# Kernel optimization log

Measured on AMD Instinct MI355X. Metric: run time of the kernel, lower is better.

Reference implementation:

```python
import jax, jax.numpy as jnp
import numpy as np

HEADS = 4


def rel_to_abs(x):
    """Convert relative logits [..., L, 2L-1] to absolute [..., L, L].
    out[..., i, j] = x[..., i, j - i + L - 1]."""
    L = x.shape[-2]
    idx = jnp.arange(L)[None, :] - jnp.arange(L)[:, None] + (L - 1)  # [L, L]
    idx = jnp.broadcast_to(idx, x.shape[:-1] + (L,))
    return jnp.take_along_axis(x, idx, axis=-1)


def setup_inputs() -> dict:
    key = jax.random.key(0)
    ks = jax.random.split(key, 5)
    b, c, h, w = 2, 256, 64, 64
    dh = c // HEADS
    return {
        "x": jax.random.normal(ks[0], (b, c, h, w), jnp.float32),
        "w_qkv": jax.random.normal(ks[1], (3 * c, c), jnp.float32) / np.float32(np.sqrt(c)),
        "w_out": jax.random.normal(ks[2], (c, c), jnp.float32) / np.float32(np.sqrt(c)),
        "rel_height": jax.random.normal(ks[3], (2 * h - 1, dh), jnp.float32),
        "rel_width": jax.random.normal(ks[4], (2 * w - 1, dh), jnp.float32),
    }


def reference(x, w_qkv, w_out, rel_height, rel_width):
    b, c, h, w = x.shape
    dh = c // HEADS
    N = h * w
    scale = dh ** -0.5

    # 1x1 conv == per-pixel matmul over channels
    qkv = jnp.einsum('bchw,oc->bohw', x, w_qkv)  # [b, 3c, h, w]
    q, k, v = jnp.split(qkv, 3, axis=1)

    def to_heads(t):  # [b, c, h, w] -> [b, H, N, dh]
        return t.reshape(b, HEADS, dh, N).transpose(0, 1, 3, 2)

    q = to_heads(q) * scale
    k = to_heads(k)
    v = to_heads(v)

    # content-content scores over spatial positions
    content = jnp.einsum('bnid,bnjd->bnij', q, k)  # [b, H, N, N]

    q5 = q.reshape(b, HEADS, h, w, dh)  # [b, H, x, y, dh]
    # width relative logits: [b,H,x,y,2w-1] -> abs -> [b,H,x,y,jw]
    rw = rel_to_abs(jnp.einsum('bnxyd,rd->bnxyr', q5, rel_width))
    # height relative logits on transposed spatial: [b,H,y,x,2h-1] -> [b,H,y,x,jh]
    rh = rel_to_abs(jnp.einsum('bnyxd,rd->bnyxr', q5.transpose(0, 1, 3, 2, 4), rel_height))

    logits = content.reshape(b, HEADS, h, w, h, w)
    logits = logits + rw[:, :, :, :, None, :]  # broadcast width bias over target height jh
    logits = logits + rh.transpose(0, 1, 3, 2, 4)[:, :, :, :, :, None]  # [b,H,x,y,jh] over jw

    attn = jax.nn.softmax(logits.reshape(b, HEADS, N, N), axis=-1)
    out = jnp.einsum('bnij,bnjd->bnid', attn, v)  # [b, H, N, dh]
    out = out.transpose(0, 1, 3, 2).reshape(b, c, h, w)
    out = jnp.einsum('bchw,oc->bohw', out, w_out)  # 1x1 out projection
    return out + x
```

## Files before the change

### kernel.cpp

```cpp
#include <hip/hip_runtime.h>

typedef unsigned short u16;
typedef unsigned int u32;
typedef __bf16 bf16x8 __attribute__((ext_vector_type(8)));
typedef __bf16 bf16x2 __attribute__((ext_vector_type(2)));
typedef float f32x4 __attribute__((ext_vector_type(4)));
typedef float f32x2 __attribute__((ext_vector_type(2)));
typedef u32 u32x4 __attribute__((ext_vector_type(4)));
typedef u32 u32x2 __attribute__((ext_vector_type(2)));
typedef short s16x4 __attribute__((ext_vector_type(4)));

#define DEVI __device__ __forceinline__

#if defined(__has_builtin)
#if __has_builtin(__builtin_amdgcn_exp2f)
#define EXP2F(x) __builtin_amdgcn_exp2f(x)
#endif
#endif
#ifndef EXP2F
#define EXP2F(x) exp2f(x)
#endif

#define MFMA16(a, b, c) __builtin_amdgcn_mfma_f32_16x16x32_bf16(a, b, c, 0, 0, 0)
#define MFMA1K(a, b, c) __builtin_amdgcn_mfma_f32_16x16x16bf16_1k(a, b, c, 0, 0, 0)

DEVI u16 f2bf(float f) {
    u32 u = __builtin_bit_cast(u32, f);
    u = (u + 0x7FFFu + ((u >> 16) & 1u)) >> 16;
    return (u16)u;
}
DEVI float bf2f(u16 h) {
    u32 u = ((u32)h) << 16;
    return __builtin_bit_cast(float, u);
}
DEVI float bfhi(u32 u) { return __builtin_bit_cast(float, u & 0xFFFF0000u); }
DEVI float bflo(u32 u) { return __builtin_bit_cast(float, u << 16); }
DEVI bf16x8 bc8(u32x4 u) { return __builtin_bit_cast(bf16x8, u); }
DEVI u32 pack2(float a, float b) {
    f32x2 v = {a, b};
    bf16x2 h = __builtin_convertvector(v, bf16x2);
    return __builtin_bit_cast(u32, h);
}

#define QSCALE 0.18033688011112042f

__global__ __launch_bounds__(256) void k_prep(const float* __restrict__ x,
                                              const float* __restrict__ wq,
                                              const float* __restrict__ wo,
                                              const float* __restrict__ relh,
                                              const float* __restrict__ relw,
                                              u16* __restrict__ xt, u16* __restrict__ wqb,
                                              u16* __restrict__ wob, u16* __restrict__ relhb,
                                              u16* __restrict__ relwb) {
    int bid = blockIdx.x;
    int t = threadIdx.x;
    if (bid < 512) {
        int pm = bid & 63, cm = (bid >> 6) & 3, b = bid >> 8;
        int p0 = pm * 64, c0 = cm * 64;
        __shared__ float tile[64][65];
#pragma unroll
        for (int it = 0; it < 16; ++it) {
            int idx = it * 256 + t;
            int cl = idx >> 6, pl = idx & 63;
            tile[cl][pl] = x[((size_t)(b * 256 + c0 + cl)) * 4096 + p0 + pl];
        }
        __syncthreads();
#pragma unroll
        for (int it = 0; it < 16; ++it) {
            int idx = it * 256 + t;
            int pl = idx >> 6, cl = idx & 63;
            xt[((size_t)(b * 4096 + p0 + pl)) * 256 + c0 + cl] = f2bf(tile[cl][pl]);
        }
    } else {
        int i0 = (bid - 512) * 256 + t;
#pragma unroll
        for (int i = i0; i < 196608; i += 65536) wqb[i] = f2bf(wq[i]);
        if (i0 < 65536) wob[i0] = f2bf(wo[i0]);
        if (i0 < 8192) {
            relhb[i0] = (i0 < 8128) ? f2bf(relh[i0]) : (u16)0;
            relwb[i0] = (i0 < 8128) ? f2bf(relw[i0]) : (u16)0;
        }
    }
}

__global__ __launch_bounds__(256) void k_qkv(const u16* __restrict__ xt, const u16* __restrict__ wqb,
                                             u16* __restrict__ q, u16* __restrict__ k,
                                             u16* __restrict__ vt) {
    int pm = blockIdx.x, on = blockIdx.y, b = blockIdx.z;
    int p0 = pm * 64, o0 = on * 64;
    __shared__ __align__(16) u16 Bt[64 * 264];
    int t = threadIdx.x;
    int wv = t >> 6, l = t & 63, quad = l >> 4, li = l & 15;

    u32x4 areg[8];
    const u32x4* arow = (const u32x4*)(xt + ((size_t)(b * 4096 + p0 + wv * 16 + li)) * 256);
#pragma unroll
    for (int kc = 0; kc < 8; ++kc) areg[kc] = arow[kc * 4 + quad];

    {
        int row = t >> 2, c0 = (t & 3) * 64;
        const u32x4* g = (const u32x4*)(wqb + (size_t)(o0 + row) * 256 + c0);
        u32x4* s = (u32x4*)(Bt + row * 264 + c0);
#pragma unroll
        for (int kk = 0; kk < 8; ++kk) s[kk] = g[kk];
    }
    __syncthreads();

    f32x4 acc[4] = {{0, 0, 0, 0}, {0, 0, 0, 0}, {0, 0, 0, 0}, {0, 0, 0, 0}};
#pragma unroll
    for (int kc = 0; kc < 8; ++kc) {
        bf16x8 a = bc8(areg[kc]);
#pragma unroll
        for (int ct = 0; ct < 4; ++ct) {
            bf16x8 bb = bc8(*(const u32x4*)(Bt + (ct * 16 + li) * 264 + kc * 32 + quad * 8));
            acc[ct] = MFMA16(a, bb, acc[ct]);
        }
    }

    int tensor = on >> 2, head = on & 3;
    if (tensor == 2) {
        __syncthreads();
        u16* T = Bt;
#pragma unroll
        for (int ct = 0; ct < 4; ++ct)
#pragma unroll
            for (int r = 0; r < 4; ++r)
                T[(ct * 16 + li) * 72 + wv * 16 + quad * 4 + r] = f2bf(acc[ct][r]);
        __syncthreads();
        int dr = t >> 2, pc = (t & 3) * 16;
        u32x4* g = (u32x4*)(vt + ((size_t)((b * 4 + head) * 64 + dr)) * 4096 + p0 + pc);
        const u32x4* s2 = (const u32x4*)(T + dr * 72 + pc);
        g[0] = s2[0];
        g[1] = s2[1];
    } else {
        u16* outp = (tensor == 0) ? q : k;
        float sc = (tensor == 0) ? QSCALE : 1.0f;
#pragma unroll
        for (int ct = 0; ct < 4; ++ct)
#pragma unroll
            for (int r = 0; r < 4; ++r) {
                int p = p0 + wv * 16 + quad * 4 + r;
                int d = ct * 16 + li;
                outp[((size_t)((b * 4 + head) * 4096 + p)) * 64 + d] = f2bf(acc[ct][r] * sc);
            }
    }
}

__global__ __launch_bounds__(256) void k_rel(const u16* __restrict__ q,
                                             const u16* __restrict__ relwb,
                                             const u16* __restrict__ relhb,
                                             u16* __restrict__ Wabs, u16* __restrict__ Habs) {
    int pm = blockIdx.x, bh = blockIdx.y, z = blockIdx.z;
    int p0 = pm * 64;
    const u16* rel = z ? relhb : relwb;
    u16* outp = z ? Habs : Wabs;
    __shared__ __align__(16) u16 Ls[128 * 72];
    int t = threadIdx.x, wv = t >> 6, l = t & 63, quad = l >> 4, li = l & 15;

    {
        int row = t >> 1, half = t & 1;
        const u32x4* g = (const u32x4*)(rel + row * 64 + half * 32);
        u32x4* s = (u32x4*)(Ls + row * 72 + half * 32);
#pragma unroll
        for (int kk = 0; kk < 4; ++kk) s[kk] = g[kk];
    }

    u32x4 aq[2];
    const u32x4* qrow = (const u32x4*)(q + ((size_t)(bh * 4096 + p0 + wv * 16 + li)) * 64);
    aq[0] = qrow[quad];
    aq[1] = qrow[4 + quad];
    __syncthreads();

    f32x4 acc[8];
#pragma unroll
    for (int ct = 0; ct < 8; ++ct) acc[ct] = (f32x4){0.f, 0.f, 0.f, 0.f};
#pragma unroll
    for (int kc = 0; kc < 2; ++kc) {
        bf16x8 a = bc8(aq[kc]);
#pragma unroll
        for (int ct = 0; ct < 8; ++ct) {
            bf16x8 bb = bc8(*(const u32x4*)(Ls + (ct * 16 + li) * 72 + kc * 32 + quad * 8));
            acc[ct] = MFMA16(a, bb, acc[ct]);
        }
    }

#pragma unroll
    for (int ct = 0; ct < 8; ++ct)
#pragma unroll
        for (int r = 0; r < 4; ++r) {
            int row = wv * 16 + quad * 4 + r;
            int p = p0 + row;
            int c = ct * 16 + li;
            int shift = z ? pm : row;
            int j = c - 63 + shift;
            if (j >= 0 && j < 64)
                outp[((size_t)(bh * 4096 + p)) * 64 + j] = f2bf(acc[ct][r]);
        }
}

__global__ __launch_bounds__(256, 2) void k_flash(const u16* __restrict__ q,
                                                  const u16* __restrict__ kg,
                                                  const u16* __restrict__ vt,
                                                  const u16* __restrict__ Wabs,
                                                  const u16* __restrict__ Habs,
                                                  u16* __restrict__ OP,
                                                  float* __restrict__ LS) {
    int pm = blockIdx.x, bh = blockIdx.y, ks = blockIdx.z;
    int p0 = pm * 128;
    __shared__ __align__(16) u16 Kt[2][64 * 72];
    __shared__ __align__(16) u16 Vl[2][64 * 72];
    __shared__ __align__(16) u16 Hl[128 * 40];
    int t = threadIdx.x, wv = t >> 6, l = t & 63, quad = l >> 4, li = l & 15;
    int rbase = wv * 32;

    u32x4 aq[2][2];
#pragma unroll
    for (int rs = 0; rs < 2; ++rs) {
        const u32x4* qrow =
            (const u32x4*)(q + ((size_t)(bh * 4096 + p0 + rbase + rs * 16 + li)) * 64);
        aq[rs][0] = qrow[quad];
        aq[rs][1] = qrow[4 + quad];
    }

    f32x4 wb4[2][4];
#pragma unroll
    for (int rs = 0; rs < 2; ++rs)
#pragma unroll
        for (int ct = 0; ct < 4; ++ct) {
            const u32* wp = (const u32*)(Wabs +
                                         ((size_t)(bh * 4096 + p0 + rbase + rs * 16 + li)) * 64 +
                                         ct * 16 + quad * 4);
            u32 lo = wp[0], hi = wp[1];
            wb4[rs][ct] = (f32x4){bflo(lo), bfhi(lo), bflo(hi), bfhi(hi)};
        }

    {
        int row = t >> 1, ch = (t & 1) * 16;
        const u32x4* g = (const u32x4*)(Habs + ((size_t)(bh * 4096 + p0 + row)) * 64 + ks * 32 + ch);
        u32x4* d = (u32x4*)(Hl + row * 40 + ch);
        d[0] = g[0];
        d[1] = g[1];
    }

    int srow = t >> 2, scc = (t & 3) * 16;
    {
        int j0 = ks * 2048;
        const u32x4* gk = (const u32x4*)(kg + ((size_t)(bh * 4096 + j0 + srow)) * 64 + scc);
        u32x4* sk = (u32x4*)(Kt[0] + srow * 72 + scc);
        sk[0] = gk[0];
        sk[1] = gk[1];
        const u32x4* gv = (const u32x4*)(vt + ((size_t)(bh * 64 + srow)) * 4096 + j0 + scc);
        u32x4* sv = (u32x4*)(Vl[0] + srow * 72 + scc);
        sv[0] = gv[0];
        sv[1] = gv[1];
    }

    f32x4 oacc[2][5];
#pragma unroll
    for (int rs = 0; rs < 2; ++rs)
#pragma unroll
        for (int ct = 0; ct < 5; ++ct) oacc[rs][ct] = (f32x4){0.f, 0.f, 0.f, 0.f};

    const s16x4 ones = {(short)0x3F80, (short)0x3F80, (short)0x3F80, (short)0x3F80};

    u32x4 kreg[2], vreg[2];
    for (int kt = 0; kt < 32; ++kt) {
        __syncthreads();
        int cur = kt & 1;
        const u16* Kc = Kt[cur];
        const u16* Vc = Vl[cur];
        if (kt < 31) {
            int j0 = (ks * 32 + kt + 1) * 64;
            const u32x4* gk = (const u32x4*)(kg + ((size_t)(bh * 4096 + j0 + srow)) * 64 + scc);
            kreg[0] = gk[0];
            kreg[1] = gk[1];
            const u32x4* gv = (const u32x4*)(vt + ((size_t)(bh * 64 + srow)) * 4096 + j0 + scc);
            vreg[0] = gv[0];
            vreg[1] = gv[1];
        }

        float hh0 = bf2f(Hl[(rbase + li) * 40 + kt]);
        float hh1 = bf2f(Hl[(rbase + 16 + li) * 40 + kt]);
        f32x4 s[2][4];
#pragma unroll
        for (int ct = 0; ct < 4; ++ct) {
            s[0][ct] = wb4[0][ct] + hh0;
            s[1][ct] = wb4[1][ct] + hh1;
        }
#pragma unroll
        for (int kc = 0; kc < 2; ++kc) {
            bf16x8 b0 = bc8(aq[0][kc]), b1 = bc8(aq[1][kc]);
#pragma unroll
            for (int ct = 0; ct < 4; ++ct) {
                bf16x8 af = bc8(*(const u32x4*)(Kc + (ct * 16 + li) * 72 + kc * 32 + quad * 8));
                s[0][ct] = MFMA16(af, b0, s[0][ct]);
                s[1][ct] = MFMA16(af, b1, s[1][ct]);
            }
        }

        s16x4 pf[2][4];
#pragma unroll
        for (int rs = 0; rs < 2; ++rs)
#pragma unroll
            for (int ct = 0; ct < 4; ++ct) {
                u32x2 pp;
                pp.x = pack2(EXP2F(s[rs][ct][0]), EXP2F(s[rs][ct][1]));
                pp.y = pack2(EXP2F(s[rs][ct][2]), EXP2F(s[rs][ct][3]));
                pf[rs][ct] = __builtin_bit_cast(s16x4, pp);
            }

#pragma unroll
        for (int jt = 0; jt < 4; ++jt) {
            s16x4 a0 = pf[0][jt], a1 = pf[1][jt];
#pragma unroll
            for (int dt = 0; dt < 4; ++dt) {
                s16x4 bv = __builtin_bit_cast(
                    s16x4, *(const u32x2*)(Vc + (dt * 16 + li) * 72 + jt * 16 + quad * 4));
                oacc[0][dt] = MFMA1K(a0, bv, oacc[0][dt]);
                oacc[1][dt] = MFMA1K(a1, bv, oacc[1][dt]);
            }
            oacc[0][4] = MFMA1K(a0, ones, oacc[0][4]);
            oacc[1][4] = MFMA1K(a1, ones, oacc[1][4]);
        }

        if (kt < 31) {
            u32x4* sk = (u32x4*)(Kt[cur ^ 1] + srow * 72 + scc);
            sk[0] = kreg[0];
            sk[1] = kreg[1];
            u32x4* sv = (u32x4*)(Vl[cur ^ 1] + srow * 72 + scc);
            sv[0] = vreg[0];
            sv[1] = vreg[1];
        }
    }

#pragma unroll
    for (int rs = 0; rs < 2; ++rs) {
#pragma unroll
        for (int ct = 0; ct < 4; ++ct)
#pragma unroll
            for (int r = 0; r < 4; ++r) {
                int p = p0 + rbase + rs * 16 + quad * 4 + r;
                OP[((size_t)((ks * 8 + bh) * 4096 + p)) * 64 + ct * 16 + li] =
                    f2bf(oacc[rs][ct][r]);
            }
        if (li == 0) {
#pragma unroll
            for (int r = 0; r < 4; ++r) {
                int p = p0 + rbase + rs * 16 + quad * 4 + r;
                LS[(size_t)(ks * 8 + bh) * 4096 + p] = oacc[rs][4][r];
            }
        }
    }
}

__global__ __launch_bounds__(256) void k_out2(const u16* __restrict__ wob,
                                              const u16* __restrict__ OP,
                                              const float* __restrict__ LS,
                                              const float* __restrict__ x,
                                              float* __restrict__ out) {
    int pm = blockIdx.x, b = blockIdx.y, coh = blockIdx.z;
    int p0 = pm * 64;
    __shared__ __align__(16) u16 Bt[64 * 264];
    int t = threadIdx.x, wv = t >> 6, l = t & 63, quad = l >> 4, li = l & 15;

    {
        int row = t >> 2, head = t & 3;
        int bh = b * 4 + head;
        int p = p0 + row;
        const u32x4* o0p = (const u32x4*)(OP + ((size_t)(bh * 4096 + p)) * 64);
        const u32x4* o1p = (const u32x4*)(OP + ((size_t)((8 + bh) * 4096 + p)) * 64);
        float linv = 1.0f / (LS[(size_t)bh * 4096 + p] + LS[(size_t)(8 + bh) * 4096 + p]);
        u16* dst = Bt + row * 264 + head * 64;
#pragma unroll
        for (int kk = 0; kk < 8; ++kk) {
            u32x4 a = o0p[kk], c = o1p[kk];
            u32x4 pk;
            pk.x = pack2((bflo(a.x) + bflo(c.x)) * linv, (bfhi(a.x) + bfhi(c.x)) * linv);
            pk.y = pack2((bflo(a.y) + bflo(c.y)) * linv, (bfhi(a.y) + bfhi(c.y)) * linv);
            pk.z = pack2((bflo(a.z) + bflo(c.z)) * linv, (bfhi(a.z) + bfhi(c.z)) * linv);
            pk.w = pack2((bflo(a.w) + bflo(c.w)) * linv, (bfhi(a.w) + bfhi(c.w)) * linv);
            *(u32x4*)(dst + kk * 8) = pk;
        }
    }
    __syncthreads();

#pragma unroll
    for (int ci = 0; ci < 2; ++ci) {
        int com = coh * 2 + ci;
        int co0 = com * 64;
        f32x4 acc[4] = {{0, 0, 0, 0}, {0, 0, 0, 0}, {0, 0, 0, 0}, {0, 0, 0, 0}};
        const u32x4* arow = (const u32x4*)(wob + (size_t)(co0 + wv * 16 + li) * 256);
#pragma unroll
        for (int kc = 0; kc < 8; ++kc) {
            bf16x8 a = bc8(arow[kc * 4 + quad]);
#pragma unroll
            for (int ct = 0; ct < 4; ++ct) {
                bf16x8 bb = bc8(*(const u32x4*)(Bt + (ct * 16 + li) * 264 + kc * 32 + quad * 8));
                acc[ct] = MFMA16(a, bb, acc[ct]);
            }
        }
#pragma unroll
        for (int ct = 0; ct < 4; ++ct)
#pragma unroll
            for (int r = 0; r < 4; ++r) {
                size_t idx =
                    ((size_t)(b * 256 + co0 + wv * 16 + quad * 4 + r)) * 4096 + p0 + ct * 16 + li;
                out[idx] = acc[ct][r] + x[idx];
            }
    }
}

extern "C" void kernel_launch(void* const* d_in, const int* in_sizes, int n_in, void* d_out,
                              int out_size, void* d_ws, size_t ws_size, hipStream_t stream) {
    const float* x = (const float*)d_in[0];
    const float* wqkv = (const float*)d_in[1];
    const float* wout = (const float*)d_in[2];
    const float* relh = (const float*)d_in[3];
    const float* relw = (const float*)d_in[4];
    float* out = (float*)d_out;
    char* ws = (char*)d_ws;

    u16* xt = (u16*)(ws + 0);
    u16* wqb = (u16*)(ws + 4194304);
    u16* wob = (u16*)(ws + 4587520);
    u16* relwb = (u16*)(ws + 4718592);
    u16* relhb = (u16*)(ws + 4734976);
    u16* qb = (u16*)(ws + 4751360);
    u16* kb = (u16*)(ws + 8945664);
    u16* vtb = (u16*)(ws + 13139968);
    u16* Wabs = (u16*)(ws + 17334272);
    u16* Habs = (u16*)(ws + 21528576);
    u16* OPart = (u16*)(ws + 25722880);
    float* LSum = (float*)(ws + 34111488);

    k_prep<<<768, 256, 0, stream>>>(x, wqkv, wout, relh, relw, xt, wqb, wob, relhb, relwb);
    k_qkv<<<dim3(64, 12, 2), 256, 0, stream>>>(xt, wqb, qb, kb, vtb);
    k_rel<<<dim3(64, 8, 2), 256, 0, stream>>>(qb, relwb, relhb, Wabs, Habs);
    k_flash<<<dim3(32, 8, 2), 256, 0, stream>>>(qb, kb, vtb, Wabs, Habs, OPart, LSum);
    k_out2<<<dim3(64, 2, 2), 256, 0, stream>>>(wob, OPart, LSum, x, out);
}
```

Measured before the change: 152.6 us.

## Fuse rel-logit GEMMs into QKV kernel and split flash keys four ways

```diff
diff --git a/kernel.cpp b/kernel.cpp
--- a/kernel.cpp
+++ b/kernel.cpp
@@ -84,8 +84,11 @@
 }
 
 __global__ __launch_bounds__(256) void k_qkv(const u16* __restrict__ xt, const u16* __restrict__ wqb,
+                                             const u16* __restrict__ relwb,
+                                             const u16* __restrict__ relhb,
                                              u16* __restrict__ q, u16* __restrict__ k,
-                                             u16* __restrict__ vt) {
+                                             u16* __restrict__ vt, u16* __restrict__ Wabs,
+                                             u16* __restrict__ Habs) {
     int pm = blockIdx.x, on = blockIdx.y, b = blockIdx.z;
     int p0 = pm * 64, o0 = on * 64;
     __shared__ __align__(16) u16 Bt[64 * 264];
@@ -143,59 +146,80 @@
                 int d = ct * 16 + li;
                 outp[((size_t)((b * 4 + head) * 4096 + p)) * 64 + d] = f2bf(acc[ct][r] * sc);
             }
-    }
-}
-
-__global__ __launch_bounds__(256) void k_rel(const u16* __restrict__ q,
-                                             const u16* __restrict__ relwb,
-                                             const u16* __restrict__ relhb,
-                                             u16* __restrict__ Wabs, u16* __restrict__ Habs) {
-    int pm = blockIdx.x, bh = blockIdx.y, z = blockIdx.z;
-    int p0 = pm * 64;
-    const u16* rel = z ? relhb : relwb;
-    u16* outp = z ? Habs : Wabs;
-    __shared__ __align__(16) u16 Ls[128 * 72];
-    int t = threadIdx.x, wv = t >> 6, l = t & 63, quad = l >> 4, li = l & 15;
-
-    {
-        int row = t >> 1, half = t & 1;
-        const u32x4* g = (const u32x4*)(rel + row * 64 + half * 32);
-        u32x4* s = (u32x4*)(Ls + row * 72 + half * 32);
-#pragma unroll
-        for (int kk = 0; kk < 4; ++kk) s[kk] = g[kk];
-    }
-
-    u32x4 aq[2];
-    const u32x4* qrow = (const u32x4*)(q + ((size_t)(bh * 4096 + p0 + wv * 16 + li)) * 64);
-    aq[0] = qrow[quad];
-    aq[1] = qrow[4 + quad];
-    __syncthreads();
-
-    f32x4 acc[8];
-#pragma unroll
-    for (int ct = 0; ct < 8; ++ct) acc[ct] = (f32x4){0.f, 0.f, 0.f, 0.f};
-#pragma unroll
-    for (int kc = 0; kc < 2; ++kc) {
-        bf16x8 a = bc8(aq[kc]);
-#pragma unroll
-        for (int ct = 0; ct < 8; ++ct) {
-            bf16x8 bb = bc8(*(const u32x4*)(Ls + (ct * 16 + li) * 72 + kc * 32 + quad * 8));
-            acc[ct] = MFMA16(a, bb, acc[ct]);
-        }
-    }
-
-#pragma unroll
-    for (int ct = 0; ct < 8; ++ct)
-#pragma unroll
-        for (int r = 0; r < 4; ++r) {
-            int row = wv * 16 + quad * 4 + r;
-            int p = p0 + row;
-            int c = ct * 16 + li;
-            int shift = z ? pm : row;
-            int j = c - 63 + shift;
-            if (j >= 0 && j < 64)
-                outp[((size_t)(bh * 4096 + p)) * 64 + j] = f2bf(acc[ct][r]);
-        }
+        if (tensor == 0) {
+            int bh = b * 4 + head;
+            u16* T = Bt;
+            u16* Ls = Bt + 64 * 72;
+            __syncthreads();
+#pragma unroll
+            for (int ct = 0; ct < 4; ++ct)
+#pragma unroll
+                for (int r = 0; r < 4; ++r)
+                    T[(wv * 16 + quad * 4 + r) * 72 + ct * 16 + li] = f2bf(acc[ct][r] * QSCALE);
+            {
+                int row = t >> 1, half = t & 1;
+                const u32x4* g2 = (const u32x4*)(relwb + row * 64 + half * 32);
+                u32x4* s2 = (u32x4*)(Ls + row * 72 + half * 32);
+#pragma unroll
+                for (int kk = 0; kk < 4; ++kk) s2[kk] = g2[kk];
+            }
+            __syncthreads();
+            u32x4 aq2[2];
+            aq2[0] = *(const u32x4*)(T + (wv * 16 + li) * 72 + quad * 8);
+            aq2[1] = *(const u32x4*)(T + (wv * 16 + li) * 72 + 32 + quad * 8);
+
+            f32x4 acc2[8];
+#pragma unroll
+            for (int ct = 0; ct < 8; ++ct) acc2[ct] = (f32x4){0.f, 0.f, 0.f, 0.f};
+#pragma unroll
+            for (int kc = 0; kc < 2; ++kc) {
+                bf16x8 a = bc8(aq2[kc]);
+#pragma unroll
+                for (int ct = 0; ct < 8; ++ct) {
+                    bf16x8 bb = bc8(*(const u32x4*)(Ls + (ct * 16 + li) * 72 + kc * 32 + quad * 8));
+                    acc2[ct] = MFMA16(a, bb, acc2[ct]);
+                }
+            }
+#pragma unroll
+            for (int ct = 0; ct < 8; ++ct)
+#pragma unroll
+                for (int r = 0; r < 4; ++r) {
+                    int row = wv * 16 + quad * 4 + r;
+                    int j = (ct * 16 + li) - 63 + row;
+                    if (j >= 0 && j < 64)
+                        Wabs[((size_t)(bh * 4096 + p0 + row)) * 64 + j] = f2bf(acc2[ct][r]);
+                }
+            __syncthreads();
+            {
+                int row = t >> 1, half = t & 1;
+                const u32x4* g2 = (const u32x4*)(relhb + row * 64 + half * 32);
+                u32x4* s2 = (u32x4*)(Ls + row * 72 + half * 32);
+#pragma unroll
+                for (int kk = 0; kk < 4; ++kk) s2[kk] = g2[kk];
+            }
+            __syncthreads();
+#pragma unroll
+            for (int ct = 0; ct < 8; ++ct) acc2[ct] = (f32x4){0.f, 0.f, 0.f, 0.f};
+#pragma unroll
+            for (int kc = 0; kc < 2; ++kc) {
+                bf16x8 a = bc8(aq2[kc]);
+#pragma unroll
+                for (int ct = 0; ct < 8; ++ct) {
+                    bf16x8 bb = bc8(*(const u32x4*)(Ls + (ct * 16 + li) * 72 + kc * 32 + quad * 8));
+                    acc2[ct] = MFMA16(a, bb, acc2[ct]);
+                }
+            }
+#pragma unroll
+            for (int ct = 0; ct < 8; ++ct)
+#pragma unroll
+                for (int r = 0; r < 4; ++r) {
+                    int row = wv * 16 + quad * 4 + r;
+                    int j = (ct * 16 + li) - 63 + pm;
+                    if (j >= 0 && j < 64)
+                        Habs[((size_t)(bh * 4096 + p0 + row)) * 64 + j] = f2bf(acc2[ct][r]);
+                }
+        }
+    }
 }
 
 __global__ __launch_bounds__(256, 2) void k_flash(const u16* __restrict__ q,
@@ -209,7 +233,7 @@
     int p0 = pm * 128;
     __shared__ __align__(16) u16 Kt[2][64 * 72];
     __shared__ __align__(16) u16 Vl[2][64 * 72];
-    __shared__ __align__(16) u16 Hl[128 * 40];
+    __shared__ __align__(16) u16 Hl[128 * 24];
     int t = threadIdx.x, wv = t >> 6, l = t & 63, quad = l >> 4, li = l & 15;
     int rbase = wv * 32;
 
@@ -235,16 +259,15 @@
         }
 
     {
-        int row = t >> 1, ch = (t & 1) * 16;
-        const u32x4* g = (const u32x4*)(Habs + ((size_t)(bh * 4096 + p0 + row)) * 64 + ks * 32 + ch);
-        u32x4* d = (u32x4*)(Hl + row * 40 + ch);
-        d[0] = g[0];
-        d[1] = g[1];
+        int row = t >> 1, half = t & 1;
+        const u32x4* g =
+            (const u32x4*)(Habs + ((size_t)(bh * 4096 + p0 + row)) * 64 + ks * 16 + half * 8);
+        *(u32x4*)(Hl + row * 24 + half * 8) = g[0];
     }
 
     int srow = t >> 2, scc = (t & 3) * 16;
     {
-        int j0 = ks * 2048;
+        int j0 = ks * 1024;
         const u32x4* gk = (const u32x4*)(kg + ((size_t)(bh * 4096 + j0 + srow)) * 64 + scc);
         u32x4* sk = (u32x4*)(Kt[0] + srow * 72 + scc);
         sk[0] = gk[0];
@@ -264,13 +287,13 @@
     const s16x4 ones = {(short)0x3F80, (short)0x3F80, (short)0x3F80, (short)0x3F80};
 
     u32x4 kreg[2], vreg[2];
-    for (int kt = 0; kt < 32; ++kt) {
+    for (int kt = 0; kt < 16; ++kt) {
         __syncthreads();
         int cur = kt & 1;
         const u16* Kc = Kt[cur];
         const u16* Vc = Vl[cur];
-        if (kt < 31) {
-            int j0 = (ks * 32 + kt + 1) * 64;
+        if (kt < 15) {
+            int j0 = (ks * 16 + kt + 1) * 64;
             const u32x4* gk = (const u32x4*)(kg + ((size_t)(bh * 4096 + j0 + srow)) * 64 + scc);
             kreg[0] = gk[0];
             kreg[1] = gk[1];
@@ -279,8 +302,8 @@
             vreg[1] = gv[1];
         }
 
-        float hh0 = bf2f(Hl[(rbase + li) * 40 + kt]);
-        float hh1 = bf2f(Hl[(rbase + 16 + li) * 40 + kt]);
+        float hh0 = bf2f(Hl[(rbase + li) * 24 + kt]);
+        float hh1 = bf2f(Hl[(rbase + 16 + li) * 24 + kt]);
         f32x4 s[2][4];
 #pragma unroll
         for (int ct = 0; ct < 4; ++ct) {
@@ -323,7 +346,7 @@
             oacc[1][4] = MFMA1K(a1, ones, oacc[1][4]);
         }
 
-        if (kt < 31) {
+        if (kt < 15) {
             u32x4* sk = (u32x4*)(Kt[cur ^ 1] + srow * 72 + scc);
             sk[0] = kreg[0];
             sk[1] = kreg[1];
@@ -358,7 +381,7 @@
                                               const float* __restrict__ LS,
                                               const float* __restrict__ x,
                                               float* __restrict__ out) {
-    int pm = blockIdx.x, b = blockIdx.y, coh = blockIdx.z;
+    int pm = blockIdx.x, b = blockIdx.y, com = blockIdx.z;
     int p0 = pm * 64;
     __shared__ __align__(16) u16 Bt[64 * 264];
     int t = threadIdx.x, wv = t >> 6, l = t & 63, quad = l >> 4, li = l & 15;
@@ -367,47 +390,52 @@
         int row = t >> 2, head = t & 3;
         int bh = b * 4 + head;
         int p = p0 + row;
-        const u32x4* o0p = (const u32x4*)(OP + ((size_t)(bh * 4096 + p)) * 64);
-        const u32x4* o1p = (const u32x4*)(OP + ((size_t)((8 + bh) * 4096 + p)) * 64);
-        float linv = 1.0f / (LS[(size_t)bh * 4096 + p] + LS[(size_t)(8 + bh) * 4096 + p]);
+        const u32x4* op[4];
+        float lsum = 0.f;
+#pragma unroll
+        for (int s2 = 0; s2 < 4; ++s2) {
+            op[s2] = (const u32x4*)(OP + ((size_t)((s2 * 8 + bh) * 4096 + p)) * 64);
+            lsum += LS[(size_t)(s2 * 8 + bh) * 4096 + p];
+        }
+        float linv = 1.0f / lsum;
         u16* dst = Bt + row * 264 + head * 64;
 #pragma unroll
         for (int kk = 0; kk < 8; ++kk) {
-            u32x4 a = o0p[kk], c = o1p[kk];
+            u32x4 a = op[0][kk], c = op[1][kk], e = op[2][kk], f = op[3][kk];
             u32x4 pk;
-            pk.x = pack2((bflo(a.x) + bflo(c.x)) * linv, (bfhi(a.x) + bfhi(c.x)) * linv);
-            pk.y = pack2((bflo(a.y) + bflo(c.y)) * linv, (bfhi(a.y) + bfhi(c.y)) * linv);
-            pk.z = pack2((bflo(a.z) + bflo(c.z)) * linv, (bfhi(a.z) + bfhi(c.z)) * linv);
-            pk.w = pack2((bflo(a.w) + bflo(c.w)) * linv, (bfhi(a.w) + bfhi(c.w)) * linv);
+            pk.x = pack2((bflo(a.x) + bflo(c.x) + bflo(e.x) + bflo(f.x)) * linv,
+                         (bfhi(a.x) + bfhi(c.x) + bfhi(e.x) + bfhi(f.x)) * linv);
+            pk.y = pack2((bflo(a.y) + bflo(c.y) + bflo(e.y) + bflo(f.y)) * linv,
+                         (bfhi(a.y) + bfhi(c.y) + bfhi(e.y) + bfhi(f.y)) * linv);
+            pk.z = pack2((bflo(a.z) + bflo(c.z) + bflo(e.z) + bflo(f.z)) * linv,
+                         (bfhi(a.z) + bfhi(c.z) + bfhi(e.z) + bfhi(f.z)) * linv);
+            pk.w = pack2((bflo(a.w) + bflo(c.w) + bflo(e.w) + bflo(f.w)) * linv,
+                         (bfhi(a.w) + bfhi(c.w) + bfhi(e.w) + bfhi(f.w)) * linv);
             *(u32x4*)(dst + kk * 8) = pk;
         }
     }
     __syncthreads();
 
-#pragma unroll
-    for (int ci = 0; ci < 2; ++ci) {
-        int com = coh * 2 + ci;
-        int co0 = com * 64;
-        f32x4 acc[4] = {{0, 0, 0, 0}, {0, 0, 0, 0}, {0, 0, 0, 0}, {0, 0, 0, 0}};
-        const u32x4* arow = (const u32x4*)(wob + (size_t)(co0 + wv * 16 + li) * 256);
-#pragma unroll
-        for (int kc = 0; kc < 8; ++kc) {
-            bf16x8 a = bc8(arow[kc * 4 + quad]);
-#pragma unroll
-            for (int ct = 0; ct < 4; ++ct) {
-                bf16x8 bb = bc8(*(const u32x4*)(Bt + (ct * 16 + li) * 264 + kc * 32 + quad * 8));
-                acc[ct] = MFMA16(a, bb, acc[ct]);
-            }
-        }
-#pragma unroll
-        for (int ct = 0; ct < 4; ++ct)
-#pragma unroll
-            for (int r = 0; r < 4; ++r) {
-                size_t idx =
-                    ((size_t)(b * 256 + co0 + wv * 16 + quad * 4 + r)) * 4096 + p0 + ct * 16 + li;
-                out[idx] = acc[ct][r] + x[idx];
-            }
-    }
+    int co0 = com * 64;
+    f32x4 acc[4] = {{0, 0, 0, 0}, {0, 0, 0, 0}, {0, 0, 0, 0}, {0, 0, 0, 0}};
+    const u32x4* arow = (const u32x4*)(wob + (size_t)(co0 + wv * 16 + li) * 256);
+#pragma unroll
+    for (int kc = 0; kc < 8; ++kc) {
+        bf16x8 a = bc8(arow[kc * 4 + quad]);
+#pragma unroll
+        for (int ct = 0; ct < 4; ++ct) {
+            bf16x8 bb = bc8(*(const u32x4*)(Bt + (ct * 16 + li) * 264 + kc * 32 + quad * 8));
+            acc[ct] = MFMA16(a, bb, acc[ct]);
+        }
+    }
+#pragma unroll
+    for (int ct = 0; ct < 4; ++ct)
+#pragma unroll
+        for (int r = 0; r < 4; ++r) {
+            size_t idx =
+                ((size_t)(b * 256 + co0 + wv * 16 + quad * 4 + r)) * 4096 + p0 + ct * 16 + li;
+            out[idx] = acc[ct][r] + x[idx];
+        }
 }
 
 extern "C" void kernel_launch(void* const* d_in, const int* in_sizes, int n_in, void* d_out,
@@ -431,11 +459,10 @@
     u16* Wabs = (u16*)(ws + 17334272);
     u16* Habs = (u16*)(ws + 21528576);
     u16* OPart = (u16*)(ws + 25722880);
-    float* LSum = (float*)(ws + 34111488);
+    float* LSum = (float*)(ws + 0);
 
     k_prep<<<768, 256, 0, stream>>>(x, wqkv, wout, relh, relw, xt, wqb, wob, relhb, relwb);
-    k_qkv<<<dim3(64, 12, 2), 256, 0, stream>>>(xt, wqb, qb, kb, vtb);
-    k_rel<<<dim3(64, 8, 2), 256, 0, stream>>>(qb, relwb, relhb, Wabs, Habs);
-    k_flash<<<dim3(32, 8, 2), 256, 0, stream>>>(qb, kb, vtb, Wabs, Habs, OPart, LSum);
-    k_out2<<<dim3(64, 2, 2), 256, 0, stream>>>(wob, OPart, LSum, x, out);
-}
+    k_qkv<<<dim3(64, 12, 2), 256, 0, stream>>>(xt, wqb, relwb, relhb, qb, kb, vtb, Wabs, Habs);
+    k_flash<<<dim3(32, 8, 4), 256, 0, stream>>>(qb, kb, vtb, Wabs, Habs, OPart, LSum);
+    k_out2<<<dim3(64, 2, 4), 256, 0, stream>>>(wob, OPart, LSum, x, out);
+}
```

Measured after the change: 153.6 us. Within noise of the previous version (+0.6%).
